# Optimization experiments

Hardware: AMD Instinct MI355X
Metric: run time of the kernel (lower is better)

## Reference

```python
import jax, jax.numpy as jnp
import numpy as np

HIDDEN = 1024
HEADS = 16
HEAD_DIM = HIDDEN // HEADS          # 64
ROT = 2 * (HEAD_DIM // 3 // 2)      # 20 (d/h/w rotary chunk), residual = 4
GRID = 256 // 16                    # crop_size // patch_size = 16
DEPTH = 16 // 2                     # frames_per_clip // tubelet_size = 8
N_VIDEO = DEPTH * GRID * GRID       # 2048
N_ACTION = 16
B = 2
SCALE = HEAD_DIM ** -0.5


def _rope(x, pos):
    # interleaved RoPE (VJEPA2 rotate_queries_or_keys): pairs (x[2i], x[2i+1])
    D = x.shape[-1]
    omega = 1.0 / (10000.0 ** (jnp.arange(D // 2, dtype=x.dtype) / (D / 2.0)))
    freq = pos.astype(x.dtype)[..., None] * omega          # (N, D/2)
    cos, sin = jnp.cos(freq), jnp.sin(freq)
    x1, x2 = x[..., 0::2], x[..., 1::2]
    return jnp.stack([x1 * cos - x2 * sin, x2 * cos + x1 * sin], axis=-1).reshape(x.shape)


def _rope3(qk, d_pos, h_pos, w_pos):
    # rotate three ROT-sized chunks (depth/height/width axes), leave residual dims as-is
    parts = [_rope(qk[..., 0:ROT], d_pos),
             _rope(qk[..., ROT:2 * ROT], h_pos),
             _rope(qk[..., 2 * ROT:3 * ROT], w_pos)]
    if 3 * ROT < HEAD_DIM:
        parts.append(qk[..., 3 * ROT:])
    return jnp.concatenate(parts, axis=-1)


def _forward(video_hidden_states, action_hidden_states, W_q, b_q, W_k, b_k, W_v, b_v,
             W_qa, b_qa, W_ka, b_ka, W_va, b_va, W_proj, b_proj, W_proj_a, b_proj_a):
    Bsz, Nv, _ = video_hidden_states.shape
    Na = action_hidden_states.shape[1]

    def proj(x, W, b):  # -> (B, H, N, Dh)
        y = x @ W.T + b
        return y.reshape(Bsz, -1, HEADS, HEAD_DIM).transpose(0, 2, 1, 3)

    qv = proj(video_hidden_states, W_q, b_q)
    kv = proj(video_hidden_states, W_k, b_k)
    vv = proj(video_hidden_states, W_v, b_v)

    # 3-axis position ids for raster-ordered video tokens
    ids = jnp.arange(Nv)
    tpf = GRID * GRID
    d_pos = ids // tpf
    rem = ids - tpf * d_pos
    h_pos = rem // GRID
    w_pos = rem - GRID * h_pos

    qv = _rope3(qv, d_pos, h_pos, w_pos)
    kv = _rope3(kv, d_pos, h_pos, w_pos)

    qa = proj(action_hidden_states, W_qa, b_qa)
    ka = proj(action_hidden_states, W_ka, b_ka)
    va = proj(action_hidden_states, W_va, b_va)

    # actions: linspace between frame-id of token 0 and token 1 (faithful to source)
    a_pos = jnp.linspace(d_pos[0].astype(jnp.float32), d_pos[1].astype(jnp.float32), Na)
    qa = _rope3(qa, a_pos, a_pos, a_pos)
    ka = _rope3(ka, a_pos, a_pos, a_pos)

    # joint attention over concatenated video+action token sequence
    q = jnp.concatenate([qv, qa], axis=2)
    k = jnp.concatenate([kv, ka], axis=2)
    v = jnp.concatenate([vv, va], axis=2)

    scores = jnp.einsum('bhqd,bhkd->bhqk', q, k) * SCALE
    probs = jax.nn.softmax(scores, axis=-1)
    ctx = jnp.einsum('bhqk,bhkd->bhqd', probs, v)
    ctx = ctx.transpose(0, 2, 1, 3).reshape(Bsz, Nv + Na, HIDDEN)

    out_video = ctx[:, :Nv] @ W_proj.T + b_proj
    out_action = ctx[:, Nv:] @ W_proj_a.T + b_proj_a
    return out_video, out_action


def setup_inputs() -> dict:
    key = jax.random.key(0)
    ks = jax.random.split(key, 12)
    sd = HIDDEN ** -0.5
    inp = {}
    for i, n in enumerate(['q', 'k', 'v', 'qa', 'ka', 'va', 'proj', 'proj_a']):
        inp[f'W_{n}'] = jax.random.normal(ks[i], (HIDDEN, HIDDEN), jnp.float32) * sd
        inp[f'b_{n}'] = jnp.zeros((HIDDEN,), jnp.float32)
    inp['video_hidden_states'] = jax.random.normal(ks[10], (B, N_VIDEO, HIDDEN), jnp.float32)
    inp['action_hidden_states'] = jax.random.normal(ks[11], (B, N_ACTION, HIDDEN), jnp.float32)
    return inp


def reference(video_hidden_states, action_hidden_states, W_q, b_q, W_k, b_k, W_v, b_v,
              W_qa, b_qa, W_ka, b_ka, W_va, b_va, W_proj, b_proj, W_proj_a, b_proj_a):
    return _forward(video_hidden_states, action_hidden_states, W_q, b_q, W_k, b_k, W_v, b_v,
                    W_qa, b_qa, W_ka, b_ka, W_va, b_va, W_proj, b_proj, W_proj_a, b_proj_a)
```

## Files before the change

kernel.cpp:

```cpp
#include <hip/hip_runtime.h>
#include <stdint.h>

#define HID   1024
#define NHEAD 16
#define HDIM  64
#define NV    2048
#define NA    16
#define NTOK  2064
#define BSZ   2
#define MROWS 4128
#define WSZ   1048576
#define EXP_C1 0.18033688011112042f
#define EXP_C2 16.0f

typedef __bf16 bf16x8 __attribute__((ext_vector_type(8)));
typedef unsigned short u16x8 __attribute__((ext_vector_type(8)));
typedef unsigned short u16x4 __attribute__((ext_vector_type(4)));
typedef float f32x4 __attribute__((ext_vector_type(4)));

__device__ __forceinline__ unsigned short f2bf(float f) {
  unsigned u = __builtin_bit_cast(unsigned, f);
  u += 0x7FFFu + ((u >> 16) & 1u);
  return (unsigned short)(u >> 16);
}
__device__ __forceinline__ unsigned short f2bf_trunc(float f) {
  return (unsigned short)(__builtin_bit_cast(unsigned, f) >> 16);
}
__device__ __forceinline__ void async_copy16(const void* g, void* l) {
  __builtin_amdgcn_global_load_lds(
      (const __attribute__((address_space(1))) unsigned int*)g,
      (__attribute__((address_space(3))) unsigned int*)l, 16, 0, 0);
}

__global__ __launch_bounds__(256) void cvt_kernel(
    const float* __restrict__ W0, const float* __restrict__ W1,
    const float* __restrict__ W2, const float* __restrict__ W3,
    const float* __restrict__ W4, const float* __restrict__ W5,
    const float* __restrict__ W6, const float* __restrict__ W7,
    const float* __restrict__ video, const float* __restrict__ action,
    unsigned short* __restrict__ Wb, unsigned short* __restrict__ Xb)
{
  const int y = blockIdx.y;
  const size_t idx = ((size_t)blockIdx.x * 256 + threadIdx.x) * 8;
  const float* src; unsigned short* dst;
  if      (y == 0)  { src = W0; dst = Wb; }
  else if (y == 1)  { src = W1; dst = Wb + 1 * WSZ; }
  else if (y == 2)  { src = W2; dst = Wb + 2 * WSZ; }
  else if (y == 3)  { src = W3; dst = Wb + 3 * WSZ; }
  else if (y == 4)  { src = W4; dst = Wb + 4 * WSZ; }
  else if (y == 5)  { src = W5; dst = Wb + 5 * WSZ; }
  else if (y == 6)  { src = W6; dst = Wb + 6 * WSZ; }
  else if (y == 7)  { src = W7; dst = Wb + 7 * WSZ; }
  else if (y < 12)  { src = video + (size_t)(y - 8) * WSZ; dst = Xb + (size_t)(y - 8) * WSZ; }
  else              { if (idx >= (size_t)BSZ * NA * HID) return;
                      src = action; dst = Xb + (size_t)4096 * HID; }
  float4 f0 = *(const float4*)(src + idx);
  float4 f1 = *(const float4*)(src + idx + 4);
  u16x8 v;
  v[0]=f2bf(f0.x); v[1]=f2bf(f0.y); v[2]=f2bf(f0.z); v[3]=f2bf(f0.w);
  v[4]=f2bf(f1.x); v[5]=f2bf(f1.y); v[6]=f2bf(f1.z); v[7]=f2bf(f1.w);
  *(u16x8*)(dst + idx) = v;
}

__device__ __forceinline__ void row2bt(int rg, int& b, int& tok, bool& valid) {
  if (rg < 4096) { b = rg >> 11; tok = rg & 2047; valid = true; }
  else { int t = rg - 4096; b = t >> 4; tok = 2048 + (t & 15); valid = rg < MROWS; }
}

__global__ __launch_bounds__(256) void qkv128_kernel(
    const unsigned short* __restrict__ Xb, const unsigned short* __restrict__ Wb,
    const float* __restrict__ bq, const float* __restrict__ bk,
    const float* __restrict__ bv, const float* __restrict__ bqa,
    const float* __restrict__ bka, const float* __restrict__ bva,
    unsigned short* __restrict__ Qo, unsigned short* __restrict__ Ko,
    unsigned short* __restrict__ Vt)
{
  __shared__ unsigned short As[128 * 32];
  __shared__ unsigned short Bs[128 * 32];

  const int tid  = threadIdx.x;
  const int w    = tid >> 6;
  const int l    = tid & 63;
  const int quad = l >> 4;
  const int l16  = l & 15;
  const int lrow = l >> 2;
  const int lk   = (l & 3) * 8;
  const int z    = blockIdx.z;
  const int m0   = blockIdx.y * 128;
  const int n0   = blockIdx.x * 128;
  const bool atile = (blockIdx.y == 32);

  const unsigned short* Wm = Wb + (size_t)(atile ? 3 + z : z) * WSZ;
  const float* bias = (z == 0) ? (atile ? bqa : bq)
                    : (z == 1) ? (atile ? bka : bk)
                               : (atile ? bva : bv);

  const int am = (w & 1) * 64;
  const int bn = (w >> 1) * 64;

  f32x4 acc[4][4] = {};

  for (int kt = 0; kt < HID; kt += 32) {
    __syncthreads();
#pragma unroll
    for (int i = 0; i < 2; i++) {
      int trow = w * 32 + i * 16;
      int arow = min(m0 + trow + lrow, MROWS - 1);
      async_copy16(Xb + (size_t)arow * HID + kt + lk, &As[trow * 32]);
      async_copy16(Wm + (size_t)(n0 + trow + lrow) * HID + kt + lk, &Bs[trow * 32]);
    }
    __syncthreads();

    bf16x8 af[4], bf[4];
#pragma unroll
    for (int mi = 0; mi < 4; mi++)
      af[mi] = __builtin_bit_cast(bf16x8, *(const u16x8*)&As[(am + mi * 16 + l16) * 32 + quad * 8]);
#pragma unroll
    for (int ni = 0; ni < 4; ni++)
      bf[ni] = __builtin_bit_cast(bf16x8, *(const u16x8*)&Bs[(bn + ni * 16 + l16) * 32 + quad * 8]);
#pragma unroll
    for (int mi = 0; mi < 4; mi++)
#pragma unroll
      for (int ni = 0; ni < 4; ni++)
        acc[mi][ni] = __builtin_amdgcn_mfma_f32_16x16x32_bf16(af[mi], bf[ni], acc[mi][ni], 0, 0, 0);
  }

  if (z < 2) {
    unsigned short* O = (z == 0) ? Qo : Ko;
#pragma unroll
    for (int mi = 0; mi < 4; mi++) {
      const int rgb = m0 + am + mi * 16 + quad * 4;
#pragma unroll
      for (int ni = 0; ni < 4; ni++) {
        const int gcol = n0 + bn + ni * 16 + l16;
        const int head = gcol >> 6, col = gcol & 63;
        const float bias_v = bias[gcol];
        const int seg = (col >= 40) ? 2 : (col >= 20) ? 1 : 0;
        const int tin = col - seg * 20;
        const float om = exp2f(-(float)(tin >> 1) * 1.3287712379549449f);
        const bool evn = !(tin & 1);
#pragma unroll
        for (int r = 0; r < 4; r++) {
          int rg = rgb + r;
          int b, tok; bool valid;
          row2bt(rg, b, tok, valid);
          float val = acc[mi][ni][r] + bias_v;
          float part = __shfl_xor(val, 1);
          if (tok < 2048 && col < 60) {
            int dp = tok >> 8, hp = (tok >> 4) & 15, wp = tok & 15;
            float pos = (seg == 0) ? (float)dp : (seg == 1) ? (float)hp : (float)wp;
            float fr = pos * om;
            float cs = cosf(fr), sn = sinf(fr);
            val = evn ? (val * cs - part * sn) : (val * cs + part * sn);
          }
          if (valid)
            O[(((size_t)b * NHEAD + head) * NTOK + tok) * HDIM + col] = f2bf(val);
        }
      }
    }
  } else {
#pragma unroll
    for (int mi = 0; mi < 4; mi++) {
      const int rgb = m0 + am + mi * 16 + quad * 4;
      int b, tok; bool valid;
      row2bt(rgb, b, tok, valid);
#pragma unroll
      for (int ni = 0; ni < 4; ni++) {
        const int gcol = n0 + bn + ni * 16 + l16;
        const int head = gcol >> 6, d = gcol & 63;
        const float bias_v = bias[gcol];
        u16x4 pk;
#pragma unroll
        for (int r = 0; r < 4; r++) pk[r] = f2bf(acc[mi][ni][r] + bias_v);
        if (valid)
          *(u16x4*)&Vt[(((size_t)b * NHEAD + head) * HDIM + d) * NTOK + tok] = pk;
      }
    }
  }
}

__global__ __launch_bounds__(256) void attn_kernel(
    const unsigned short* __restrict__ Q,
    const unsigned short* __restrict__ K,
    const unsigned short* __restrict__ Vt,
    unsigned short* __restrict__ ctx)
{
  __shared__ unsigned short Qs[64][72];
  __shared__ unsigned short Ks[64][72];
  __shared__ unsigned short Vts[64][72];
  __shared__ unsigned short Ps[4][16][68];

  const int tid  = threadIdx.x;
  const int wave = tid >> 6;
  const int lane = tid & 63;
  const int quad = lane >> 4;
  const int l16  = lane & 15;
  const int bh   = blockIdx.y;
  const int q0   = blockIdx.x * 64;
  const unsigned short* Qp  = Q  + (size_t)bh * NTOK * HDIM;
  const unsigned short* Kp  = K  + (size_t)bh * NTOK * HDIM;
  const unsigned short* Vtp = Vt + (size_t)bh * HDIM * NTOK;

  const int r  = tid >> 2;
  const int c0 = (tid & 3) * 8;

  {
    int row = min(q0 + r, NTOK - 1);
#pragma unroll
    for (int cc = 0; cc < 2; cc++) {
      int c = c0 + cc * 32;
      *(u16x8*)&Qs[r][c] = *(const u16x8*)(Qp + (size_t)row * HDIM + c);
    }
  }

  u16x8 ones_u;
#pragma unroll
  for (int i = 0; i < 8; i++) ones_u[i] = 0x3F80;
  const bf16x8 ones = __builtin_bit_cast(bf16x8, ones_u);

  f32x4 oacc[4] = {};
  f32x4 lacc = {};

  for (int kv0 = 0; kv0 < NTOK; kv0 += 64) {
    __syncthreads();
    {
      int row = min(kv0 + r, NTOK - 1);
#pragma unroll
      for (int cc = 0; cc < 2; cc++) {
        int c = c0 + cc * 32;
        *(u16x8*)&Ks[r][c]  = *(const u16x8*)(Kp + (size_t)row * HDIM + c);
        *(u16x8*)&Vts[r][c] = *(const u16x8*)(Vtp + (size_t)r * NTOK + kv0 + c);
      }
    }
    __syncthreads();

    f32x4 sacc[4] = {};
#pragma unroll
    for (int kq = 0; kq < 64; kq += 32) {
      bf16x8 a = __builtin_bit_cast(bf16x8, *(const u16x8*)&Qs[wave * 16 + l16][kq + quad * 8]);
#pragma unroll
      for (int nt = 0; nt < 4; nt++) {
        bf16x8 bb = __builtin_bit_cast(bf16x8, *(const u16x8*)&Ks[nt * 16 + l16][kq + quad * 8]);
        sacc[nt] = __builtin_amdgcn_mfma_f32_16x16x32_bf16(a, bb, sacc[nt], 0, 0, 0);
      }
    }

#pragma unroll
    for (int nt = 0; nt < 4; nt++) {
      bool valid = (kv0 + nt * 16 + l16) < NTOK;
#pragma unroll
      for (int rr = 0; rr < 4; rr++) {
        float p = exp2f(__builtin_fmaf(sacc[nt][rr], EXP_C1, -EXP_C2));
        p = valid ? p : 0.f;
        Ps[wave][quad * 4 + rr][nt * 16 + l16] = f2bf_trunc(p);
      }
    }

#pragma unroll
    for (int kq = 0; kq < 64; kq += 32) {
      u16x4 alo = *(const u16x4*)&Ps[wave][l16][kq + quad * 8];
      u16x4 ahi = *(const u16x4*)&Ps[wave][l16][kq + quad * 8 + 4];
      bf16x8 a = __builtin_bit_cast(bf16x8,
          __builtin_shufflevector(alo, ahi, 0, 1, 2, 3, 4, 5, 6, 7));
#pragma unroll
      for (int nt = 0; nt < 4; nt++) {
        bf16x8 bb = __builtin_bit_cast(bf16x8, *(const u16x8*)&Vts[nt * 16 + l16][kq + quad * 8]);
        oacc[nt] = __builtin_amdgcn_mfma_f32_16x16x32_bf16(a, bb, oacc[nt], 0, 0, 0);
      }
      lacc = __builtin_amdgcn_mfma_f32_16x16x32_bf16(a, ones, lacc, 0, 0, 0);
    }
  }

  const int b = bh >> 4, h = bh & 15;
  float rl[4];
#pragma unroll
  for (int rr = 0; rr < 4; rr++) rl[rr] = 1.f / lacc[rr];
#pragma unroll
  for (int nt = 0; nt < 4; nt++) {
#pragma unroll
    for (int rr = 0; rr < 4; rr++) {
      int token = q0 + wave * 16 + quad * 4 + rr;
      if (token < NTOK) {
        int row = (token < 2048) ? (b * 2048 + token) : (4096 + b * NA + (token - 2048));
        int d = nt * 16 + l16;
        ctx[(size_t)row * HID + h * HDIM + d] = f2bf(oacc[nt][rr] * rl[rr]);
      }
    }
  }
}

__global__ __launch_bounds__(256) void proj128_kernel(
    const unsigned short* __restrict__ ctx, const unsigned short* __restrict__ Wb,
    const float* __restrict__ bp, const float* __restrict__ bpa,
    float* __restrict__ out)
{
  __shared__ unsigned short As[128 * 32];
  __shared__ unsigned short Bs[128 * 32];

  const int tid  = threadIdx.x;
  const int w    = tid >> 6;
  const int l    = tid & 63;
  const int quad = l >> 4;
  const int l16  = l & 15;
  const int lrow = l >> 2;
  const int lk   = (l & 3) * 8;
  const int m0   = blockIdx.y * 128;
  const int n0   = blockIdx.x * 128;
  const bool atile = (blockIdx.y == 32);

  const unsigned short* Wm = Wb + (size_t)(atile ? 7 : 6) * WSZ;
  const float* bias = atile ? bpa : bp;

  const int am = (w & 1) * 64;
  const int bn = (w >> 1) * 64;

  f32x4 acc[4][4] = {};

  for (int kt = 0; kt < HID; kt += 32) {
    __syncthreads();
#pragma unroll
    for (int i = 0; i < 2; i++) {
      int trow = w * 32 + i * 16;
      int arow = min(m0 + trow + lrow, MROWS - 1);
      async_copy16(ctx + (size_t)arow * HID + kt + lk, &As[trow * 32]);
      async_copy16(Wm + (size_t)(n0 + trow + lrow) * HID + kt + lk, &Bs[trow * 32]);
    }
    __syncthreads();

    bf16x8 af[4], bf[4];
#pragma unroll
    for (int mi = 0; mi < 4; mi++)
      af[mi] = __builtin_bit_cast(bf16x8, *(const u16x8*)&As[(am + mi * 16 + l16) * 32 + quad * 8]);
#pragma unroll
    for (int ni = 0; ni < 4; ni++)
      bf[ni] = __builtin_bit_cast(bf16x8, *(const u16x8*)&Bs[(bn + ni * 16 + l16) * 32 + quad * 8]);
#pragma unroll
    for (int mi = 0; mi < 4; mi++)
#pragma unroll
      for (int ni = 0; ni < 4; ni++)
        acc[mi][ni] = __builtin_amdgcn_mfma_f32_16x16x32_bf16(af[mi], bf[ni], acc[mi][ni], 0, 0, 0);
  }

#pragma unroll
  for (int mi = 0; mi < 4; mi++) {
    const int rgb = m0 + am + mi * 16 + quad * 4;
#pragma unroll
    for (int ni = 0; ni < 4; ni++) {
      const int gcol = n0 + bn + ni * 16 + l16;
      const float bias_v = bias[gcol];
#pragma unroll
      for (int r = 0; r < 4; r++) {
        int rg = rgb + r;
        if (rg < MROWS) out[(size_t)rg * HID + gcol] = acc[mi][ni][r] + bias_v;
      }
    }
  }
}

extern "C" void kernel_launch(void* const* d_in, const int* in_sizes, int n_in,
                              void* d_out, int out_size, void* d_ws, size_t ws_size,
                              hipStream_t stream) {
  const float* A[18];
  if (in_sizes[0] == HID * HID) {
    for (int i = 0; i < 18; i++) A[i] = (const float*)d_in[i];
  } else {
    A[16] = (const float*)d_in[0];
    A[17] = (const float*)d_in[1];
    for (int i = 0; i < 16; i++) A[i] = (const float*)d_in[i + 2];
  }
  const float *Wq = A[0], *bq = A[1], *Wk = A[2], *bk = A[3], *Wv = A[4], *bv = A[5];
  const float *Wqa = A[6], *bqa = A[7], *Wka = A[8], *bka = A[9], *Wva = A[10], *bva = A[11];
  const float *Wp = A[12], *bp = A[13], *Wpa = A[14], *bpa = A[15];
  const float *video = A[16], *action = A[17];
  float* out = (float*)d_out;

  const size_t qkv_elems = (size_t)BSZ * NHEAD * NTOK * HDIM;
  unsigned short* Wb  = (unsigned short*)d_ws;
  unsigned short* Xb  = Wb + (size_t)8 * WSZ;
  unsigned short* Qw  = Xb + (size_t)MROWS * HID;
  unsigned short* Kw  = Qw + qkv_elems;
  unsigned short* Vtw = Kw + qkv_elems;
  unsigned short* ctx = Vtw + qkv_elems;

  dim3 g0(512, 13);
  cvt_kernel<<<g0, 256, 0, stream>>>(Wq, Wk, Wv, Wqa, Wka, Wva, Wp, Wpa,
                                     video, action, Wb, Xb);
  dim3 g1(8, 33, 3);
  qkv128_kernel<<<g1, 256, 0, stream>>>(Xb, Wb, bq, bk, bv, bqa, bka, bva,
                                        Qw, Kw, Vtw);
  dim3 g2(33, BSZ * NHEAD);
  attn_kernel<<<g2, 256, 0, stream>>>(Qw, Kw, Vtw, ctx);
  dim3 g3(8, 33);
  proj128_kernel<<<g3, 256, 0, stream>>>(ctx, Wb, bp, bpa, out);
}
```

Baseline: 382.1 us.

## Double-buffer shared tiles in QKV, projection GEMMs and attention KV loop

The QKV and output-projection GEMMs now use two LDS buffers. The next K-slice's async copies are issued right after a single barrier, so loads for one slice overlap the MFMAs on the current one. The attention kernel likewise prefetches the next K/Vt tile into registers and writes it into an alternating LDS buffer, which removes one barrier per iteration. The cost is doubled shared memory and extra live registers, which may lower occupancy.

```diff
diff --git a/kernel.cpp b/kernel.cpp
--- a/kernel.cpp
+++ b/kernel.cpp
@@ -75,8 +75,8 @@
     unsigned short* __restrict__ Qo, unsigned short* __restrict__ Ko,
     unsigned short* __restrict__ Vt)
 {
-  __shared__ unsigned short As[128 * 32];
-  __shared__ unsigned short Bs[128 * 32];
+  __shared__ unsigned short As[2][128 * 32];
+  __shared__ unsigned short Bs[2][128 * 32];
 
   const int tid  = threadIdx.x;
   const int w    = tid >> 6;
@@ -95,29 +95,39 @@
                     : (z == 1) ? (atile ? bka : bk)
                                : (atile ? bva : bv);
 
+  const int trow0 = w * 32, trow1 = w * 32 + 16;
+  const unsigned short* pa0 = Xb + (size_t)min(m0 + trow0 + lrow, MROWS - 1) * HID + lk;
+  const unsigned short* pa1 = Xb + (size_t)min(m0 + trow1 + lrow, MROWS - 1) * HID + lk;
+  const unsigned short* pb0 = Wm + (size_t)(n0 + trow0 + lrow) * HID + lk;
+  const unsigned short* pb1 = Wm + (size_t)(n0 + trow1 + lrow) * HID + lk;
+
   const int am = (w & 1) * 64;
   const int bn = (w >> 1) * 64;
 
   f32x4 acc[4][4] = {};
 
-  for (int kt = 0; kt < HID; kt += 32) {
+  async_copy16(pa0, &As[0][trow0 * 32]);
+  async_copy16(pa1, &As[0][trow1 * 32]);
+  async_copy16(pb0, &Bs[0][trow0 * 32]);
+  async_copy16(pb1, &Bs[0][trow1 * 32]);
+
+  for (int kt = 0; kt < 32; kt++) {
+    const int cur = kt & 1;
     __syncthreads();
-#pragma unroll
-    for (int i = 0; i < 2; i++) {
-      int trow = w * 32 + i * 16;
-      int arow = min(m0 + trow + lrow, MROWS - 1);
-      async_copy16(Xb + (size_t)arow * HID + kt + lk, &As[trow * 32]);
-      async_copy16(Wm + (size_t)(n0 + trow + lrow) * HID + kt + lk, &Bs[trow * 32]);
-    }
-    __syncthreads();
-
+    if (kt < 31) {
+      const int kn = (kt + 1) * 32;
+      async_copy16(pa0 + kn, &As[cur ^ 1][trow0 * 32]);
+      async_copy16(pa1 + kn, &As[cur ^ 1][trow1 * 32]);
+      async_copy16(pb0 + kn, &Bs[cur ^ 1][trow0 * 32]);
+      async_copy16(pb1 + kn, &Bs[cur ^ 1][trow1 * 32]);
+    }
     bf16x8 af[4], bf[4];
 #pragma unroll
     for (int mi = 0; mi < 4; mi++)
-      af[mi] = __builtin_bit_cast(bf16x8, *(const u16x8*)&As[(am + mi * 16 + l16) * 32 + quad * 8]);
+      af[mi] = __builtin_bit_cast(bf16x8, *(const u16x8*)&As[cur][(am + mi * 16 + l16) * 32 + quad * 8]);
 #pragma unroll
     for (int ni = 0; ni < 4; ni++)
-      bf[ni] = __builtin_bit_cast(bf16x8, *(const u16x8*)&Bs[(bn + ni * 16 + l16) * 32 + quad * 8]);
+      bf[ni] = __builtin_bit_cast(bf16x8, *(const u16x8*)&Bs[cur][(bn + ni * 16 + l16) * 32 + quad * 8]);
 #pragma unroll
     for (int mi = 0; mi < 4; mi++)
 #pragma unroll
@@ -186,8 +196,8 @@
     unsigned short* __restrict__ ctx)
 {
   __shared__ unsigned short Qs[64][72];
-  __shared__ unsigned short Ks[64][72];
-  __shared__ unsigned short Vts[64][72];
+  __shared__ unsigned short Ks[2][64][72];
+  __shared__ unsigned short Vts[2][64][72];
   __shared__ unsigned short Ps[4][16][68];
 
   const int tid  = threadIdx.x;
@@ -221,18 +231,36 @@
   f32x4 oacc[4] = {};
   f32x4 lacc = {};
 
-  for (int kv0 = 0; kv0 < NTOK; kv0 += 64) {
+  u16x8 kreg[2], vreg[2];
+  {
+    int row = min(r, NTOK - 1);
+#pragma unroll
+    for (int cc = 0; cc < 2; cc++) {
+      int c = c0 + cc * 32;
+      kreg[cc] = *(const u16x8*)(Kp + (size_t)row * HDIM + c);
+      vreg[cc] = *(const u16x8*)(Vtp + (size_t)r * NTOK + c);
+    }
+  }
+
+  for (int it = 0; it < 33; it++) {
+    const int cur = it & 1;
+    const int kv0 = it * 64;
+#pragma unroll
+    for (int cc = 0; cc < 2; cc++) {
+      int c = c0 + cc * 32;
+      *(u16x8*)&Ks[cur][r][c]  = kreg[cc];
+      *(u16x8*)&Vts[cur][r][c] = vreg[cc];
+    }
     __syncthreads();
-    {
-      int row = min(kv0 + r, NTOK - 1);
+    if (it < 32) {
+      int row = min(kv0 + 64 + r, NTOK - 1);
 #pragma unroll
       for (int cc = 0; cc < 2; cc++) {
         int c = c0 + cc * 32;
-        *(u16x8*)&Ks[r][c]  = *(const u16x8*)(Kp + (size_t)row * HDIM + c);
-        *(u16x8*)&Vts[r][c] = *(const u16x8*)(Vtp + (size_t)r * NTOK + kv0 + c);
-      }
-    }
-    __syncthreads();
+        kreg[cc] = *(const u16x8*)(Kp + (size_t)row * HDIM + c);
+        vreg[cc] = *(const u16x8*)(Vtp + (size_t)r * NTOK + kv0 + 64 + c);
+      }
+    }
 
     f32x4 sacc[4] = {};
 #pragma unroll
@@ -240,7 +268,7 @@
       bf16x8 a = __builtin_bit_cast(bf16x8, *(const u16x8*)&Qs[wave * 16 + l16][kq + quad * 8]);
 #pragma unroll
       for (int nt = 0; nt < 4; nt++) {
-        bf16x8 bb = __builtin_bit_cast(bf16x8, *(const u16x8*)&Ks[nt * 16 + l16][kq + quad * 8]);
+        bf16x8 bb = __builtin_bit_cast(bf16x8, *(const u16x8*)&Ks[cur][nt * 16 + l16][kq + quad * 8]);
         sacc[nt] = __builtin_amdgcn_mfma_f32_16x16x32_bf16(a, bb, sacc[nt], 0, 0, 0);
       }
     }
@@ -264,7 +292,7 @@
           __builtin_shufflevector(alo, ahi, 0, 1, 2, 3, 4, 5, 6, 7));
 #pragma unroll
       for (int nt = 0; nt < 4; nt++) {
-        bf16x8 bb = __builtin_bit_cast(bf16x8, *(const u16x8*)&Vts[nt * 16 + l16][kq + quad * 8]);
+        bf16x8 bb = __builtin_bit_cast(bf16x8, *(const u16x8*)&Vts[cur][nt * 16 + l16][kq + quad * 8]);
         oacc[nt] = __builtin_amdgcn_mfma_f32_16x16x32_bf16(a, bb, oacc[nt], 0, 0, 0);
       }
       lacc = __builtin_amdgcn_mfma_f32_16x16x32_bf16(a, ones, lacc, 0, 0, 0);
@@ -294,8 +322,8 @@
     const float* __restrict__ bp, const float* __restrict__ bpa,
     float* __restrict__ out)
 {
-  __shared__ unsigned short As[128 * 32];
-  __shared__ unsigned short Bs[128 * 32];
+  __shared__ unsigned short As[2][128 * 32];
+  __shared__ unsigned short Bs[2][128 * 32];
 
   const int tid  = threadIdx.x;
   const int w    = tid >> 6;
@@ -311,29 +339,39 @@
   const unsigned short* Wm = Wb + (size_t)(atile ? 7 : 6) * WSZ;
   const float* bias = atile ? bpa : bp;
 
+  const int trow0 = w * 32, trow1 = w * 32 + 16;
+  const unsigned short* pa0 = ctx + (size_t)min(m0 + trow0 + lrow, MROWS - 1) * HID + lk;
+  const unsigned short* pa1 = ctx + (size_t)min(m0 + trow1 + lrow, MROWS - 1) * HID + lk;
+  const unsigned short* pb0 = Wm + (size_t)(n0 + trow0 + lrow) * HID + lk;
+  const unsigned short* pb1 = Wm + (size_t)(n0 + trow1 + lrow) * HID + lk;
+
   const int am = (w & 1) * 64;
   const int bn = (w >> 1) * 64;
 
   f32x4 acc[4][4] = {};
 
-  for (int kt = 0; kt < HID; kt += 32) {
+  async_copy16(pa0, &As[0][trow0 * 32]);
+  async_copy16(pa1, &As[0][trow1 * 32]);
+  async_copy16(pb0, &Bs[0][trow0 * 32]);
+  async_copy16(pb1, &Bs[0][trow1 * 32]);
+
+  for (int kt = 0; kt < 32; kt++) {
+    const int cur = kt & 1;
     __syncthreads();
-#pragma unroll
-    for (int i = 0; i < 2; i++) {
-      int trow = w * 32 + i * 16;
-      int arow = min(m0 + trow + lrow, MROWS - 1);
-      async_copy16(ctx + (size_t)arow * HID + kt + lk, &As[trow * 32]);
-      async_copy16(Wm + (size_t)(n0 + trow + lrow) * HID + kt + lk, &Bs[trow * 32]);
-    }
-    __syncthreads();
-
+    if (kt < 31) {
+      const int kn = (kt + 1) * 32;
+      async_copy16(pa0 + kn, &As[cur ^ 1][trow0 * 32]);
+      async_copy16(pa1 + kn, &As[cur ^ 1][trow1 * 32]);
+      async_copy16(pb0 + kn, &Bs[cur ^ 1][trow0 * 32]);
+      async_copy16(pb1 + kn, &Bs[cur ^ 1][trow1 * 32]);
+    }
     bf16x8 af[4], bf[4];
 #pragma unroll
     for (int mi = 0; mi < 4; mi++)
-      af[mi] = __builtin_bit_cast(bf16x8, *(const u16x8*)&As[(am + mi * 16 + l16) * 32 + quad * 8]);
+      af[mi] = __builtin_bit_cast(bf16x8, *(const u16x8*)&As[cur][(am + mi * 16 + l16) * 32 + quad * 8]);
 #pragma unroll
     for (int ni = 0; ni < 4; ni++)
-      bf[ni] = __builtin_bit_cast(bf16x8, *(const u16x8*)&Bs[(bn + ni * 16 + l16) * 32 + quad * 8]);
+      bf[ni] = __builtin_bit_cast(bf16x8, *(const u16x8*)&Bs[cur][(bn + ni * 16 + l16) * 32 + quad * 8]);
 #pragma unroll
     for (int mi = 0; mi < 4; mi++)
 #pragma unroll
```

Measured after the change: 387.1 us. About the same (+1.3%).

## Pre-pack operands in MFMA fragment layout and load fragments directly from global memory

Applied to the files above, without the earlier changes.

Every intermediate buffer (X, W, Q, K, V, ctx) is now written in a fragment-packed tiled layout, so each lane can load its bf16x8 MFMA operand straight from global memory. This removes the LDS staging and __syncthreads from the GEMM and attention loops. The attention loop also drops per-tile bounds masking by handling the final partial KV tile separately. The cost is that each wave issues redundant global and L2 loads with no cross-wave sharing, and the padded layouts rely on garbage or zero padding being correct. The V accumulator index now uses an odd comma expression.

```diff
diff --git a/kernel.cpp b/kernel.cpp
--- a/kernel.cpp
+++ b/kernel.cpp
@@ -9,9 +9,16 @@
 #define NTOK  2064
 #define BSZ   2
 #define MROWS 4128
+#define MPAD  4224
 #define WSZ   1048576
 #define EXP_C1 0.18033688011112042f
 #define EXP_C2 16.0f
+
+#define POFF(r,k)  (((((r)>>4)*32  + ((k)>>5))*512) + ((((k)>>3)&3)*128) + (((r)&15)*8) + ((k)&7))
+#define QOFF(t,d)  (((((t)>>4)*2   + ((d)>>5))*512) + ((((d)>>3)&3)*128) + (((t)&15)*8) + ((d)&7))
+#define VOFF(d,ky) (((((d)>>4)*65  + ((ky)>>5))*512) + ((((ky)>>3)&3)*128) + (((d)&15)*8) + ((ky)&7))
+#define QPLANE (129*2*512)
+#define VPLANE (4*65*512)
 
 typedef __bf16 bf16x8 __attribute__((ext_vector_type(8)));
 typedef unsigned short u16x8 __attribute__((ext_vector_type(8)));
@@ -23,13 +30,14 @@
   u += 0x7FFFu + ((u >> 16) & 1u);
   return (unsigned short)(u >> 16);
 }
+__device__ __forceinline__ float bf2f_trunc_inv(unsigned short h) {
+  unsigned u = ((unsigned)h) << 16; return __builtin_bit_cast(float, u);
+}
 __device__ __forceinline__ unsigned short f2bf_trunc(float f) {
   return (unsigned short)(__builtin_bit_cast(unsigned, f) >> 16);
 }
-__device__ __forceinline__ void async_copy16(const void* g, void* l) {
-  __builtin_amdgcn_global_load_lds(
-      (const __attribute__((address_space(1))) unsigned int*)g,
-      (__attribute__((address_space(3))) unsigned int*)l, 16, 0, 0);
+__device__ __forceinline__ bf16x8 ldfrag(const unsigned short* p) {
+  return __builtin_bit_cast(bf16x8, *(const u16x8*)p);
 }
 
 __global__ __launch_bounds__(256) void cvt_kernel(
@@ -38,28 +46,28 @@
     const float* __restrict__ W4, const float* __restrict__ W5,
     const float* __restrict__ W6, const float* __restrict__ W7,
     const float* __restrict__ video, const float* __restrict__ action,
-    unsigned short* __restrict__ Wb, unsigned short* __restrict__ Xb)
+    unsigned short* __restrict__ Wb, unsigned short* __restrict__ Xp)
 {
   const int y = blockIdx.y;
   const size_t idx = ((size_t)blockIdx.x * 256 + threadIdx.x) * 8;
-  const float* src; unsigned short* dst;
-  if      (y == 0)  { src = W0; dst = Wb; }
-  else if (y == 1)  { src = W1; dst = Wb + 1 * WSZ; }
-  else if (y == 2)  { src = W2; dst = Wb + 2 * WSZ; }
-  else if (y == 3)  { src = W3; dst = Wb + 3 * WSZ; }
-  else if (y == 4)  { src = W4; dst = Wb + 4 * WSZ; }
-  else if (y == 5)  { src = W5; dst = Wb + 5 * WSZ; }
-  else if (y == 6)  { src = W6; dst = Wb + 6 * WSZ; }
-  else if (y == 7)  { src = W7; dst = Wb + 7 * WSZ; }
-  else if (y < 12)  { src = video + (size_t)(y - 8) * WSZ; dst = Xb + (size_t)(y - 8) * WSZ; }
-  else              { if (idx >= (size_t)BSZ * NA * HID) return;
-                      src = action; dst = Xb + (size_t)4096 * HID; }
-  float4 f0 = *(const float4*)(src + idx);
-  float4 f1 = *(const float4*)(src + idx + 4);
+  const float* src; unsigned short* dstbase; int row;
+  if (y < 8) {
+    const float* Ws[8] = {W0, W1, W2, W3, W4, W5, W6, W7};
+    src = Ws[y] + idx; dstbase = Wb + (size_t)y * WSZ; row = (int)(idx >> 10);
+  } else if (y < 12) {
+    src = video + (size_t)(y - 8) * WSZ + idx; dstbase = Xp;
+    row = ((y - 8) << 10) + (int)(idx >> 10);
+  } else {
+    if (idx >= (size_t)BSZ * NA * HID) return;
+    src = action + idx; dstbase = Xp; row = 4096 + (int)(idx >> 10);
+  }
+  const int k0 = (int)(idx & 1023);
+  float4 f0 = *(const float4*)src;
+  float4 f1 = *(const float4*)(src + 4);
   u16x8 v;
   v[0]=f2bf(f0.x); v[1]=f2bf(f0.y); v[2]=f2bf(f0.z); v[3]=f2bf(f0.w);
   v[4]=f2bf(f1.x); v[5]=f2bf(f1.y); v[6]=f2bf(f1.z); v[7]=f2bf(f1.w);
-  *(u16x8*)(dst + idx) = v;
+  *(u16x8*)(dstbase + POFF(row, k0)) = v;
 }
 
 __device__ __forceinline__ void row2bt(int rg, int& b, int& tok, bool& valid) {
@@ -67,57 +75,46 @@
   else { int t = rg - 4096; b = t >> 4; tok = 2048 + (t & 15); valid = rg < MROWS; }
 }
 
-__global__ __launch_bounds__(256) void qkv128_kernel(
-    const unsigned short* __restrict__ Xb, const unsigned short* __restrict__ Wb,
+__global__ __launch_bounds__(256) void qkv_kernel(
+    const unsigned short* __restrict__ Xp, const unsigned short* __restrict__ Wb,
     const float* __restrict__ bq, const float* __restrict__ bk,
     const float* __restrict__ bv, const float* __restrict__ bqa,
     const float* __restrict__ bka, const float* __restrict__ bva,
-    unsigned short* __restrict__ Qo, unsigned short* __restrict__ Ko,
-    unsigned short* __restrict__ Vt)
+    unsigned short* __restrict__ Qpk, unsigned short* __restrict__ Kpk,
+    unsigned short* __restrict__ Vpk)
 {
-  __shared__ unsigned short As[128 * 32];
-  __shared__ unsigned short Bs[128 * 32];
-
   const int tid  = threadIdx.x;
   const int w    = tid >> 6;
-  const int l    = tid & 63;
-  const int quad = l >> 4;
-  const int l16  = l & 15;
-  const int lrow = l >> 2;
-  const int lk   = (l & 3) * 8;
+  const int lane = tid & 63;
+  const int quad = lane >> 4;
+  const int l16  = lane & 15;
   const int z    = blockIdx.z;
   const int m0   = blockIdx.y * 128;
   const int n0   = blockIdx.x * 128;
   const bool atile = (blockIdx.y == 32);
 
-  const unsigned short* Wm = Wb + (size_t)(atile ? 3 + z : z) * WSZ;
+  const unsigned short* Wz = Wb + (size_t)(atile ? 3 + z : z) * WSZ;
   const float* bias = (z == 0) ? (atile ? bqa : bq)
                     : (z == 1) ? (atile ? bka : bk)
                                : (atile ? bva : bv);
 
   const int am = (w & 1) * 64;
   const int bn = (w >> 1) * 64;
+  const int Mt = (m0 >> 4) + (am >> 4);
+  const int Nt = (n0 >> 4) + (bn >> 4);
+
+  const unsigned short* pa = Xp + (size_t)Mt * 32 * 512 + lane * 8;
+  const unsigned short* pb = Wz + (size_t)Nt * 32 * 512 + lane * 8;
 
   f32x4 acc[4][4] = {};
 
-  for (int kt = 0; kt < HID; kt += 32) {
-    __syncthreads();
-#pragma unroll
-    for (int i = 0; i < 2; i++) {
-      int trow = w * 32 + i * 16;
-      int arow = min(m0 + trow + lrow, MROWS - 1);
-      async_copy16(Xb + (size_t)arow * HID + kt + lk, &As[trow * 32]);
-      async_copy16(Wm + (size_t)(n0 + trow + lrow) * HID + kt + lk, &Bs[trow * 32]);
-    }
-    __syncthreads();
-
+#pragma unroll 2
+  for (int kt = 0; kt < 32; kt++) {
     bf16x8 af[4], bf[4];
 #pragma unroll
-    for (int mi = 0; mi < 4; mi++)
-      af[mi] = __builtin_bit_cast(bf16x8, *(const u16x8*)&As[(am + mi * 16 + l16) * 32 + quad * 8]);
-#pragma unroll
-    for (int ni = 0; ni < 4; ni++)
-      bf[ni] = __builtin_bit_cast(bf16x8, *(const u16x8*)&Bs[(bn + ni * 16 + l16) * 32 + quad * 8]);
+    for (int mi = 0; mi < 4; mi++) af[mi] = ldfrag(pa + (size_t)(mi * 32 + kt) * 512);
+#pragma unroll
+    for (int ni = 0; ni < 4; ni++) bf[ni] = ldfrag(pb + (size_t)(ni * 32 + kt) * 512);
 #pragma unroll
     for (int mi = 0; mi < 4; mi++)
 #pragma unroll
@@ -126,7 +123,7 @@
   }
 
   if (z < 2) {
-    unsigned short* O = (z == 0) ? Qo : Ko;
+    unsigned short* O = (z == 0) ? Qpk : Kpk;
 #pragma unroll
     for (int mi = 0; mi < 4; mi++) {
       const int rgb = m0 + am + mi * 16 + quad * 4;
@@ -154,7 +151,7 @@
             val = evn ? (val * cs - part * sn) : (val * cs + part * sn);
           }
           if (valid)
-            O[(((size_t)b * NHEAD + head) * NTOK + tok) * HDIM + col] = f2bf(val);
+            O[(size_t)(b * NHEAD + head) * QPLANE + QOFF(tok, col)] = f2bf(val);
         }
       }
     }
@@ -171,23 +168,20 @@
         const float bias_v = bias[gcol];
         u16x4 pk;
 #pragma unroll
-        for (int r = 0; r < 4; r++) pk[r] = f2bf(acc[mi][ni][r] + bias_v);
+        for (int r = 0; r < 4; r++) pk[r] = f2bf(acc[z >= 2 ? 0 : 0, mi][ni][r] + bias_v);
         if (valid)
-          *(u16x4*)&Vt[(((size_t)b * NHEAD + head) * HDIM + d) * NTOK + tok] = pk;
+          *(u16x4*)&Vpk[(size_t)(b * NHEAD + head) * VPLANE + VOFF(d, tok)] = pk;
       }
     }
   }
 }
 
 __global__ __launch_bounds__(256) void attn_kernel(
-    const unsigned short* __restrict__ Q,
-    const unsigned short* __restrict__ K,
-    const unsigned short* __restrict__ Vt,
-    unsigned short* __restrict__ ctx)
+    const unsigned short* __restrict__ Qpk,
+    const unsigned short* __restrict__ Kpk,
+    const unsigned short* __restrict__ Vpk,
+    unsigned short* __restrict__ ctxp)
 {
-  __shared__ unsigned short Qs[64][72];
-  __shared__ unsigned short Ks[64][72];
-  __shared__ unsigned short Vts[64][72];
   __shared__ unsigned short Ps[4][16][68];
 
   const int tid  = threadIdx.x;
@@ -197,21 +191,14 @@
   const int l16  = lane & 15;
   const int bh   = blockIdx.y;
   const int q0   = blockIdx.x * 64;
-  const unsigned short* Qp  = Q  + (size_t)bh * NTOK * HDIM;
-  const unsigned short* Kp  = K  + (size_t)bh * NTOK * HDIM;
-  const unsigned short* Vtp = Vt + (size_t)bh * HDIM * NTOK;
-
-  const int r  = tid >> 2;
-  const int c0 = (tid & 3) * 8;
-
-  {
-    int row = min(q0 + r, NTOK - 1);
-#pragma unroll
-    for (int cc = 0; cc < 2; cc++) {
-      int c = c0 + cc * 32;
-      *(u16x8*)&Qs[r][c] = *(const u16x8*)(Qp + (size_t)row * HDIM + c);
-    }
-  }
+  const unsigned short* Qp = Qpk + (size_t)bh * QPLANE + lane * 8;
+  const unsigned short* Kp = Kpk + (size_t)bh * QPLANE + lane * 8;
+  const unsigned short* Vp = Vpk + (size_t)bh * VPLANE + lane * 8;
+
+  const int qt = min((q0 >> 4) + wave, 128);
+  bf16x8 aq[2];
+#pragma unroll
+  for (int c = 0; c < 2; c++) aq[c] = ldfrag(Qp + (size_t)(qt * 2 + c) * 512);
 
   u16x8 ones_u;
 #pragma unroll
@@ -221,54 +208,60 @@
   f32x4 oacc[4] = {};
   f32x4 lacc = {};
 
-  for (int kv0 = 0; kv0 < NTOK; kv0 += 64) {
-    __syncthreads();
-    {
-      int row = min(kv0 + r, NTOK - 1);
-#pragma unroll
-      for (int cc = 0; cc < 2; cc++) {
-        int c = c0 + cc * 32;
-        *(u16x8*)&Ks[r][c]  = *(const u16x8*)(Kp + (size_t)row * HDIM + c);
-        *(u16x8*)&Vts[r][c] = *(const u16x8*)(Vtp + (size_t)r * NTOK + kv0 + c);
-      }
-    }
-    __syncthreads();
-
+  for (int it = 0; it < 32; it++) {
     f32x4 sacc[4] = {};
 #pragma unroll
-    for (int kq = 0; kq < 64; kq += 32) {
-      bf16x8 a = __builtin_bit_cast(bf16x8, *(const u16x8*)&Qs[wave * 16 + l16][kq + quad * 8]);
+    for (int nt = 0; nt < 4; nt++) {
+#pragma unroll
+      for (int c = 0; c < 2; c++) {
+        bf16x8 bk = ldfrag(Kp + (size_t)((it * 4 + nt) * 2 + c) * 512);
+        sacc[nt] = __builtin_amdgcn_mfma_f32_16x16x32_bf16(aq[c], bk, sacc[nt], 0, 0, 0);
+      }
+    }
+#pragma unroll
+    for (int nt = 0; nt < 4; nt++)
+#pragma unroll
+      for (int rr = 0; rr < 4; rr++)
+        Ps[wave][quad * 4 + rr][nt * 16 + l16] =
+            f2bf_trunc(exp2f(__builtin_fmaf(sacc[nt][rr], EXP_C1, -EXP_C2)));
+
+#pragma unroll
+    for (int c = 0; c < 2; c++) {
+      u16x4 alo = *(const u16x4*)&Ps[wave][l16][c * 32 + quad * 8];
+      u16x4 ahi = *(const u16x4*)&Ps[wave][l16][c * 32 + quad * 8 + 4];
+      bf16x8 ap = __builtin_bit_cast(bf16x8,
+          __builtin_shufflevector(alo, ahi, 0, 1, 2, 3, 4, 5, 6, 7));
 #pragma unroll
       for (int nt = 0; nt < 4; nt++) {
-        bf16x8 bb = __builtin_bit_cast(bf16x8, *(const u16x8*)&Ks[nt * 16 + l16][kq + quad * 8]);
-        sacc[nt] = __builtin_amdgcn_mfma_f32_16x16x32_bf16(a, bb, sacc[nt], 0, 0, 0);
-      }
-    }
-
+        bf16x8 bv = ldfrag(Vp + (size_t)(nt * 65 + it * 2 + c) * 512);
+        oacc[nt] = __builtin_amdgcn_mfma_f32_16x16x32_bf16(ap, bv, oacc[nt], 0, 0, 0);
+      }
+      lacc = __builtin_amdgcn_mfma_f32_16x16x32_bf16(ap, ones, lacc, 0, 0, 0);
+    }
+  }
+
+  {
+    f32x4 s0 = {};
+#pragma unroll
+    for (int c = 0; c < 2; c++) {
+      bf16x8 bk = ldfrag(Kp + (size_t)(128 * 2 + c) * 512);
+      s0 = __builtin_amdgcn_mfma_f32_16x16x32_bf16(aq[c], bk, s0, 0, 0, 0);
+    }
+#pragma unroll
+    for (int rr = 0; rr < 4; rr++) {
+      Ps[wave][quad * 4 + rr][l16]      = f2bf_trunc(exp2f(__builtin_fmaf(s0[rr], EXP_C1, -EXP_C2)));
+      Ps[wave][quad * 4 + rr][16 + l16] = 0;
+    }
+    u16x4 alo = *(const u16x4*)&Ps[wave][l16][quad * 8];
+    u16x4 ahi = *(const u16x4*)&Ps[wave][l16][quad * 8 + 4];
+    bf16x8 ap = __builtin_bit_cast(bf16x8,
+        __builtin_shufflevector(alo, ahi, 0, 1, 2, 3, 4, 5, 6, 7));
 #pragma unroll
     for (int nt = 0; nt < 4; nt++) {
-      bool valid = (kv0 + nt * 16 + l16) < NTOK;
-#pragma unroll
-      for (int rr = 0; rr < 4; rr++) {
-        float p = exp2f(__builtin_fmaf(sacc[nt][rr], EXP_C1, -EXP_C2));
-        p = valid ? p : 0.f;
-        Ps[wave][quad * 4 + rr][nt * 16 + l16] = f2bf_trunc(p);
-      }
-    }
-
-#pragma unroll
-    for (int kq = 0; kq < 64; kq += 32) {
-      u16x4 alo = *(const u16x4*)&Ps[wave][l16][kq + quad * 8];
-      u16x4 ahi = *(const u16x4*)&Ps[wave][l16][kq + quad * 8 + 4];
-      bf16x8 a = __builtin_bit_cast(bf16x8,
-          __builtin_shufflevector(alo, ahi, 0, 1, 2, 3, 4, 5, 6, 7));
-#pragma unroll
-      for (int nt = 0; nt < 4; nt++) {
-        bf16x8 bb = __builtin_bit_cast(bf16x8, *(const u16x8*)&Vts[nt * 16 + l16][kq + quad * 8]);
-        oacc[nt] = __builtin_amdgcn_mfma_f32_16x16x32_bf16(a, bb, oacc[nt], 0, 0, 0);
-      }
-      lacc = __builtin_amdgcn_mfma_f32_16x16x32_bf16(a, ones, lacc, 0, 0, 0);
-    }
+      bf16x8 bv = ldfrag(Vp + (size_t)(nt * 65 + 64) * 512);
+      oacc[nt] = __builtin_amdgcn_mfma_f32_16x16x32_bf16(ap, bv, oacc[nt], 0, 0, 0);
+    }
+    lacc = __builtin_amdgcn_mfma_f32_16x16x32_bf16(ap, ones, lacc, 0, 0, 0);
   }
 
   const int b = bh >> 4, h = bh & 15;
@@ -282,58 +275,47 @@
       int token = q0 + wave * 16 + quad * 4 + rr;
       if (token < NTOK) {
         int row = (token < 2048) ? (b * 2048 + token) : (4096 + b * NA + (token - 2048));
-        int d = nt * 16 + l16;
-        ctx[(size_t)row * HID + h * HDIM + d] = f2bf(oacc[nt][rr] * rl[rr]);
-      }
-    }
-  }
-}
-
-__global__ __launch_bounds__(256) void proj128_kernel(
-    const unsigned short* __restrict__ ctx, const unsigned short* __restrict__ Wb,
+        int col = h * HDIM + nt * 16 + l16;
+        ctxp[POFF(row, col)] = f2bf(oacc[nt][rr] * rl[rr]);
+      }
+    }
+  }
+}
+
+__global__ __launch_bounds__(256) void proj_kernel(
+    const unsigned short* __restrict__ ctxp, const unsigned short* __restrict__ Wb,
     const float* __restrict__ bp, const float* __restrict__ bpa,
     float* __restrict__ out)
 {
-  __shared__ unsigned short As[128 * 32];
-  __shared__ unsigned short Bs[128 * 32];
-
   const int tid  = threadIdx.x;
   const int w    = tid >> 6;
-  const int l    = tid & 63;
-  const int quad = l >> 4;
-  const int l16  = l & 15;
-  const int lrow = l >> 2;
-  const int lk   = (l & 3) * 8;
+  const int lane = tid & 63;
+  const int quad = lane >> 4;
+  const int l16  = lane & 15;
   const int m0   = blockIdx.y * 128;
   const int n0   = blockIdx.x * 128;
   const bool atile = (blockIdx.y == 32);
 
-  const unsigned short* Wm = Wb + (size_t)(atile ? 7 : 6) * WSZ;
+  const unsigned short* Wz = Wb + (size_t)(atile ? 7 : 6) * WSZ;
   const float* bias = atile ? bpa : bp;
 
   const int am = (w & 1) * 64;
   const int bn = (w >> 1) * 64;
+  const int Mt = (m0 >> 4) + (am >> 4);
+  const int Nt = (n0 >> 4) + (bn >> 4);
+
+  const unsigned short* pa = ctxp + (size_t)Mt * 32 * 512 + lane * 8;
+  const unsigned short* pb = Wz + (size_t)Nt * 32 * 512 + lane * 8;
 
   f32x4 acc[4][4] = {};
 
-  for (int kt = 0; kt < HID; kt += 32) {
-    __syncthreads();
-#pragma unroll
-    for (int i = 0; i < 2; i++) {
-      int trow = w * 32 + i * 16;
-      int arow = min(m0 + trow + lrow, MROWS - 1);
-      async_copy16(ctx + (size_t)arow * HID + kt + lk, &As[trow * 32]);
-      async_copy16(Wm + (size_t)(n0 + trow + lrow) * HID + kt + lk, &Bs[trow * 32]);
-    }
-    __syncthreads();
-
+#pragma unroll 2
+  for (int kt = 0; kt < 32; kt++) {
     bf16x8 af[4], bf[4];
 #pragma unroll
-    for (int mi = 0; mi < 4; mi++)
-      af[mi] = __builtin_bit_cast(bf16x8, *(const u16x8*)&As[(am + mi * 16 + l16) * 32 + quad * 8]);
-#pragma unroll
-    for (int ni = 0; ni < 4; ni++)
-      bf[ni] = __builtin_bit_cast(bf16x8, *(const u16x8*)&Bs[(bn + ni * 16 + l16) * 32 + quad * 8]);
+    for (int mi = 0; mi < 4; mi++) af[mi] = ldfrag(pa + (size_t)(mi * 32 + kt) * 512);
+#pragma unroll
+    for (int ni = 0; ni < 4; ni++) bf[ni] = ldfrag(pb + (size_t)(ni * 32 + kt) * 512);
 #pragma unroll
     for (int mi = 0; mi < 4; mi++)
 #pragma unroll
@@ -374,22 +356,21 @@
   const float *video = A[16], *action = A[17];
   float* out = (float*)d_out;
 
-  const size_t qkv_elems = (size_t)BSZ * NHEAD * NTOK * HDIM;
-  unsigned short* Wb  = (unsigned short*)d_ws;
-  unsigned short* Xb  = Wb + (size_t)8 * WSZ;
-  unsigned short* Qw  = Xb + (size_t)MROWS * HID;
-  unsigned short* Kw  = Qw + qkv_elems;
-  unsigned short* Vtw = Kw + qkv_elems;
-  unsigned short* ctx = Vtw + qkv_elems;
+  unsigned short* Wb   = (unsigned short*)d_ws;
+  unsigned short* Xp   = Wb + (size_t)8 * WSZ;
+  unsigned short* Qpk  = Xp + (size_t)(MPAD / 16) * 32 * 512;
+  unsigned short* Kpk  = Qpk + (size_t)32 * QPLANE;
+  unsigned short* Vpk  = Kpk + (size_t)32 * QPLANE;
+  unsigned short* ctxp = Vpk + (size_t)32 * VPLANE;
 
   dim3 g0(512, 13);
   cvt_kernel<<<g0, 256, 0, stream>>>(Wq, Wk, Wv, Wqa, Wka, Wva, Wp, Wpa,
-                                     video, action, Wb, Xb);
+                                     video, action, Wb, Xp);
   dim3 g1(8, 33, 3);
-  qkv128_kernel<<<g1, 256, 0, stream>>>(Xb, Wb, bq, bk, bv, bqa, bka, bva,
-                                        Qw, Kw, Vtw);
+  qkv_kernel<<<g1, 256, 0, stream>>>(Xp, Wb, bq, bk, bv, bqa, bka, bva,
+                                     Qpk, Kpk, Vpk);
   dim3 g2(33, BSZ * NHEAD);
-  attn_kernel<<<g2, 256, 0, stream>>>(Qw, Kw, Vtw, ctx);
+  attn_kernel<<<g2, 256, 0, stream>>>(Qpk, Kpk, Vpk, ctxp);
   dim3 g3(8, 33);
-  proj128_kernel<<<g3, 256, 0, stream>>>(ctx, Wb, bp, bpa, out);
-}
+  proj_kernel<<<g3, 256, 0, stream>>>(ctxp, Wb, bp, bpa, out);
+}
```

Result: faster. 359.3 us (-6.0%).
